# Performance work log

Hardware: AMD Instinct MI355X
Metric: run time of the kernel (lower is better)

## Reference

```python
import jax, jax.numpy as jnp
import numpy as np

B, L, R = 4, 2048, 1024        # batch, seq_len, residual_dim
HID, EXP, K = 64, 2, 3          # hidden_dim, expansion_factor, conv_kernel_size
D = HID * EXP                   # ssm_input_dim = 128
N = HID                         # SSM state size = 64


def setup_inputs() -> dict:
    key = jax.random.key(0)
    ks = jax.random.split(key, 16)
    g = lambda k, s: jax.random.normal(k, s, dtype=jnp.float32) * 0.02
    inp = {
        "up_x":   jax.random.normal(ks[0], (B, L, R), dtype=jnp.float32),
        "W_up":   g(ks[1], (R, 2 * D)),
        "b_up":   g(ks[2], (2 * D,)),
        "conv_w": g(ks[3], (D, K)),          # depthwise Conv1d weight [C,1,K] squeezed
        "conv_b": g(ks[4], (D,)),
        "W_delta": g(ks[5], (D, D)),
        "b_delta": g(ks[6], (D,)),
        "W_B":    g(ks[7], (D, N)),
        "b_B":    g(ks[8], (N,)),
        "W_C":    g(ks[9], (D, N)),
        "b_C":    g(ks[10], (N,)),
        "A_log":  jnp.log(jnp.broadcast_to(jnp.arange(1, N + 1, dtype=jnp.float32), (D, N))),
        "D_skip": jnp.ones((D,), dtype=jnp.float32),
        "W_down": g(ks[11], (D, R)),
        "b_down": g(ks[12], (R,)),
    }
    return inp


def reference(up_x, W_up, b_up, conv_w, conv_b, W_delta, b_delta,
              W_B, b_B, W_C, b_C, A_log, D_skip, W_down, b_down):
    Lq = up_x.shape[1]
    u = up_x @ W_up + b_up                               # [B,L,2D]
    left, right = jnp.split(u, 2, axis=-1)               # each [B,L,D]

    # causal depthwise conv (pad left K-1, truncate to L)
    xp = jnp.pad(left, ((0, 0), (K - 1, 0), (0, 0)))     # [B,L+K-1,D]
    conv = sum(conv_w[:, k] * xp[:, k:k + Lq, :] for k in range(K)) + conv_b
    x = jax.nn.silu(conv)                                # [B,L,D]

    # S6 selective scan
    delta = jax.nn.softplus(x @ W_delta + b_delta)       # [B,L,D]
    Bm = x @ W_B + b_B                                   # [B,L,N]
    Cm = x @ W_C + b_C                                   # [B,L,N]
    A = -jnp.exp(A_log)                                  # [D,N]
    dA = jnp.exp(delta[..., None] * A)                   # [B,L,D,N]
    dBx = delta[..., None] * Bm[:, :, None, :] * x[..., None]  # [B,L,D,N]

    def step(h, inputs):
        dA_t, dBx_t, C_t = inputs                        # [B,D,N],[B,D,N],[B,N]
        h = dA_t * h + dBx_t
        y_t = jnp.einsum('bdn,bn->bd', h, C_t)
        return h, y_t

    h0 = jnp.zeros((up_x.shape[0], D, N), dtype=x.dtype)
    _, ys = jax.lax.scan(step, h0, (jnp.swapaxes(dA, 0, 1),
                                    jnp.swapaxes(dBx, 0, 1),
                                    jnp.swapaxes(Cm, 0, 1)))
    y = jnp.swapaxes(ys, 0, 1) + D_skip * x              # [B,L,D]

    gated = y * jax.nn.silu(right)                       # SiLU gate
    return gated @ W_down + b_down                       # [B,L,R]
```

## Files before the change

kernel.cpp:

```cpp
#include <hip/hip_runtime.h>
#include <math.h>

#define B_ 4
#define L_ 2048
#define R_ 1024
#define D_ 128
#define N_ 64
#define TWO_D 256
#define M_ (B_*L_)

#define LNC 6
#define NC 64

#define LSTR 68
#define LSTRX 136

typedef __attribute__((ext_vector_type(8))) short bf16x8;
typedef __attribute__((ext_vector_type(4))) float f32x4;

__device__ __forceinline__ float silu_f(float z) {
    return z * __builtin_amdgcn_rcpf(1.0f + __expf(-z));
}

__device__ __forceinline__ float softplus_f(float z) {
    return fmaxf(z, 0.0f) + __logf(1.0f + __expf(-fabsf(z)));
}

__device__ __forceinline__ short f2bf(float f) {
    union { float f; unsigned int u; } v; v.f = f;
    unsigned int r = v.u + 0x7FFF + ((v.u >> 16) & 1);
    return (short)(r >> 16);
}

__device__ __forceinline__ bf16x8 pack8(float4 a, float4 b) {
    bf16x8 r;
    r[0] = f2bf(a.x); r[1] = f2bf(a.y); r[2] = f2bf(a.z); r[3] = f2bf(a.w);
    r[4] = f2bf(b.x); r[5] = f2bf(b.y); r[6] = f2bf(b.z); r[7] = f2bf(b.w);
    return r;
}

__global__ __launch_bounds__(256) void gemm_up_splitk(
    const float* __restrict__ A,
    const float* __restrict__ W,
    float* __restrict__ P0,
    float* __restrict__ P1)
{
    __shared__ short Al[128 * LSTR];
    __shared__ short Bl[64 * LSTR];

    int lid = blockIdx.x;
    int xcd = lid & 7;
    int slot = lid >> 3;
    int bm = xcd * 8 + (slot >> 3);
    int r3 = slot & 7;
    int bn = r3 & 3;
    int split = r3 >> 2;
    float* P = split ? P1 : P0;
    int k0 = split * 512;

    int tid = threadIdx.x;
    int w = tid >> 6, l = tid & 63;
    int lm = l & 15, q = l >> 4;
    int wm = w * 32;

    f32x4 acc[2][4];
    #pragma unroll
    for (int i = 0; i < 2; i++)
        #pragma unroll
        for (int f = 0; f < 4; f++)
            acc[i][f] = (f32x4){0.f, 0.f, 0.f, 0.f};

    int ar = tid >> 1, ak = (tid & 1) * 16;
    int bcol = tid & 63, bk = (tid >> 6) * 8;

    const float* Ag = A + (size_t)(bm * 128 + ar) * 1024 + k0 + ak;
    const float* Wg = W + (size_t)k0 * TWO_D + (size_t)bn * 64 + bcol;

    for (int kt = 0; kt < 512; kt += 32) {
        float4 a0 = *(const float4*)(Ag + kt);
        float4 a1 = *(const float4*)(Ag + kt + 4);
        float4 a2 = *(const float4*)(Ag + kt + 8);
        float4 a3 = *(const float4*)(Ag + kt + 12);
        *(bf16x8*)&Al[ar * LSTR + ak]     = pack8(a0, a1);
        *(bf16x8*)&Al[ar * LSTR + ak + 8] = pack8(a2, a3);

        float w0 = Wg[(size_t)(kt + bk + 0) * TWO_D];
        float w1 = Wg[(size_t)(kt + bk + 1) * TWO_D];
        float w2 = Wg[(size_t)(kt + bk + 2) * TWO_D];
        float w3 = Wg[(size_t)(kt + bk + 3) * TWO_D];
        float w4 = Wg[(size_t)(kt + bk + 4) * TWO_D];
        float w5 = Wg[(size_t)(kt + bk + 5) * TWO_D];
        float w6 = Wg[(size_t)(kt + bk + 6) * TWO_D];
        float w7 = Wg[(size_t)(kt + bk + 7) * TWO_D];
        *(bf16x8*)&Bl[bcol * LSTR + bk] =
            pack8(make_float4(w0, w1, w2, w3), make_float4(w4, w5, w6, w7));

        __syncthreads();

        bf16x8 af0 = *(bf16x8*)&Al[(wm + lm) * LSTR + q * 8];
        bf16x8 af1 = *(bf16x8*)&Al[(wm + 16 + lm) * LSTR + q * 8];
        bf16x8 bfr[4];
        #pragma unroll
        for (int f = 0; f < 4; f++)
            bfr[f] = *(bf16x8*)&Bl[(f * 16 + lm) * LSTR + q * 8];

        #pragma unroll
        for (int f = 0; f < 4; f++) {
            acc[0][f] = __builtin_amdgcn_mfma_f32_16x16x32_bf16(af0, bfr[f], acc[0][f], 0, 0, 0);
            acc[1][f] = __builtin_amdgcn_mfma_f32_16x16x32_bf16(af1, bfr[f], acc[1][f], 0, 0, 0);
        }

        __syncthreads();
    }

    #pragma unroll
    for (int i = 0; i < 2; i++)
        #pragma unroll
        for (int f = 0; f < 4; f++)
            #pragma unroll
            for (int e = 0; e < 4; e++) {
                int row = bm * 128 + wm + i * 16 + q * 4 + e;
                int col = bn * 64 + f * 16 + lm;
                P[(size_t)row * TWO_D + col] = acc[i][f][e];
            }
}

__global__ __launch_bounds__(256) void convproj_mfma(
    const float* __restrict__ P0,
    const float* __restrict__ P1,
    const float* __restrict__ b_up,
    const float* __restrict__ conv_w,
    const float* __restrict__ conv_b,
    const float* __restrict__ W_delta, const float* __restrict__ b_delta,
    const float* __restrict__ W_B,     const float* __restrict__ b_B,
    const float* __restrict__ W_C,     const float* __restrict__ b_C,
    float* __restrict__ x,
    float* __restrict__ u,
    float* __restrict__ delta,
    float* __restrict__ Bm,
    float* __restrict__ Cm)
{
    __shared__ float uu[66 * 128];
    __shared__ short Xl[64 * LSTRX];
    __shared__ short Bl[64 * LSTR];

    int lid = blockIdx.x;
    int xcd = lid & 7;
    int slot = lid >> 3;
    int bm = xcd * 16 + (slot >> 2);
    int bn = slot & 3;
    int tid = threadIdx.x;

    bool seq_start = (bm & 31) == 0;

    #pragma unroll
    for (int i = 0; i < 9; i++) {
        int fi = tid + i * 256;
        if (fi < 2112) {
            int row = fi >> 5;
            int c4 = (fi & 31) * 4;
            int gr = bm * 64 + row - 2;
            float4 v;
            if (seq_start && row < 2) {
                v = make_float4(0.f, 0.f, 0.f, 0.f);
            } else {
                size_t gi = (size_t)gr * TWO_D + c4;
                float4 p0 = *(const float4*)&P0[gi];
                float4 p1 = *(const float4*)&P1[gi];
                float4 bb = *(const float4*)&b_up[c4];
                v = make_float4(p0.x + p1.x + bb.x, p0.y + p1.y + bb.y,
                                p0.z + p1.z + bb.z, p0.w + p1.w + bb.w);
            }
            *(float4*)&uu[fi * 4] = v;
        }
    }

    if (bn == 1) {
        #pragma unroll
        for (int i = 0; i < 8; i++) {
            int fi = tid + i * 256;
            int row = fi >> 5;
            int c4 = (fi & 31) * 4 + 128;
            int gr = bm * 64 + row;
            size_t gi = (size_t)gr * TWO_D + c4;
            float4 p0 = *(const float4*)&P0[gi];
            float4 p1 = *(const float4*)&P1[gi];
            float4 bb = *(const float4*)&b_up[c4];
            *(float4*)&u[gi] = make_float4(p0.x + p1.x + bb.x, p0.y + p1.y + bb.y,
                                           p0.z + p1.z + bb.z, p0.w + p1.w + bb.w);
        }
    }
    __syncthreads();

    #pragma unroll
    for (int i = 0; i < 8; i++) {
        int fi = tid + i * 256;
        int row = fi >> 5;
        int c4 = (fi & 31) * 4;
        float4 v2 = *(const float4*)&uu[(row + 2) * 128 + c4];
        float4 v1 = *(const float4*)&uu[(row + 1) * 128 + c4];
        float4 v0 = *(const float4*)&uu[(row + 0) * 128 + c4];
        float4 z;
        {
            float w0 = conv_w[(c4 + 0) * 3 + 0], w1 = conv_w[(c4 + 0) * 3 + 1], w2 = conv_w[(c4 + 0) * 3 + 2];
            z.x = silu_f(fmaf(w0, v0.x, fmaf(w1, v1.x, fmaf(w2, v2.x, conv_b[c4 + 0]))));
        }
        {
            float w0 = conv_w[(c4 + 1) * 3 + 0], w1 = conv_w[(c4 + 1) * 3 + 1], w2 = conv_w[(c4 + 1) * 3 + 2];
            z.y = silu_f(fmaf(w0, v0.y, fmaf(w1, v1.y, fmaf(w2, v2.y, conv_b[c4 + 1]))));
        }
        {
            float w0 = conv_w[(c4 + 2) * 3 + 0], w1 = conv_w[(c4 + 2) * 3 + 1], w2 = conv_w[(c4 + 2) * 3 + 2];
            z.z = silu_f(fmaf(w0, v0.z, fmaf(w1, v1.z, fmaf(w2, v2.z, conv_b[c4 + 2]))));
        }
        {
            float w0 = conv_w[(c4 + 3) * 3 + 0], w1 = conv_w[(c4 + 3) * 3 + 1], w2 = conv_w[(c4 + 3) * 3 + 2];
            z.w = silu_f(fmaf(w0, v0.w, fmaf(w1, v1.w, fmaf(w2, v2.w, conv_b[c4 + 3]))));
        }
        short4 zb;
        zb.x = f2bf(z.x); zb.y = f2bf(z.y); zb.z = f2bf(z.z); zb.w = f2bf(z.w);
        *(short4*)&Xl[row * LSTRX + c4] = zb;
        if (bn == 0) {
            int gr = bm * 64 + row;
            *(float4*)&x[(size_t)gr * D_ + c4] = z;
        }
    }

    const float* Wsel; const float* bsel; int wstride;
    if (bn < 2)       { Wsel = W_delta + bn * 64; bsel = b_delta + bn * 64; wstride = 128; }
    else if (bn == 2) { Wsel = W_B;               bsel = b_B;               wstride = 64;  }
    else              { Wsel = W_C;               bsel = b_C;               wstride = 64;  }

    int w = tid >> 6, l = tid & 63;
    int lm = l & 15, q = l >> 4;
    int wm = (w & 1) * 32, wn = (w >> 1) * 32;

    f32x4 acc00 = {0,0,0,0}, acc01 = {0,0,0,0}, acc10 = {0,0,0,0}, acc11 = {0,0,0,0};

    int bcol = tid & 63, bk = (tid >> 6) * 8;
    const float* Wg = Wsel + bcol;

    __syncthreads();

    for (int kt = 0; kt < 128; kt += 32) {
        float w0 = Wg[(size_t)(kt + bk + 0) * wstride];
        float w1 = Wg[(size_t)(kt + bk + 1) * wstride];
        float w2 = Wg[(size_t)(kt + bk + 2) * wstride];
        float w3 = Wg[(size_t)(kt + bk + 3) * wstride];
        float w4 = Wg[(size_t)(kt + bk + 4) * wstride];
        float w5 = Wg[(size_t)(kt + bk + 5) * wstride];
        float w6 = Wg[(size_t)(kt + bk + 6) * wstride];
        float w7 = Wg[(size_t)(kt + bk + 7) * wstride];
        *(bf16x8*)&Bl[bcol * LSTR + bk] =
            pack8(make_float4(w0, w1, w2, w3), make_float4(w4, w5, w6, w7));

        __syncthreads();

        bf16x8 af0 = *(bf16x8*)&Xl[(wm + lm) * LSTRX + kt + q * 8];
        bf16x8 af1 = *(bf16x8*)&Xl[(wm + 16 + lm) * LSTRX + kt + q * 8];
        bf16x8 bf0 = *(bf16x8*)&Bl[(wn + lm) * LSTR + q * 8];
        bf16x8 bf1 = *(bf16x8*)&Bl[(wn + 16 + lm) * LSTR + q * 8];

        acc00 = __builtin_amdgcn_mfma_f32_16x16x32_bf16(af0, bf0, acc00, 0, 0, 0);
        acc01 = __builtin_amdgcn_mfma_f32_16x16x32_bf16(af0, bf1, acc01, 0, 0, 0);
        acc10 = __builtin_amdgcn_mfma_f32_16x16x32_bf16(af1, bf0, acc10, 0, 0, 0);
        acc11 = __builtin_amdgcn_mfma_f32_16x16x32_bf16(af1, bf1, acc11, 0, 0, 0);

        __syncthreads();
    }

    #pragma unroll
    for (int i = 0; i < 4; i++) {
        int r0 = bm * 64 + wm + q * 4 + i;
        int r1 = r0 + 16;
        int c0 = wn + lm;
        int c1 = c0 + 16;
        float v00 = acc00[i] + bsel[c0];
        float v01 = acc01[i] + bsel[c1];
        float v10 = acc10[i] + bsel[c0];
        float v11 = acc11[i] + bsel[c1];
        if (bn < 2) {
            int cc0 = bn * 64 + c0, cc1 = bn * 64 + c1;
            delta[(size_t)r0 * D_ + cc0] = softplus_f(v00);
            delta[(size_t)r0 * D_ + cc1] = softplus_f(v01);
            delta[(size_t)r1 * D_ + cc0] = softplus_f(v10);
            delta[(size_t)r1 * D_ + cc1] = softplus_f(v11);
        } else if (bn == 2) {
            Bm[(size_t)r0 * N_ + c0] = v00;
            Bm[(size_t)r0 * N_ + c1] = v01;
            Bm[(size_t)r1 * N_ + c0] = v10;
            Bm[(size_t)r1 * N_ + c1] = v11;
        } else {
            Cm[(size_t)r0 * N_ + c0] = v00;
            Cm[(size_t)r0 * N_ + c1] = v01;
            Cm[(size_t)r1 * N_ + c0] = v10;
            Cm[(size_t)r1 * N_ + c1] = v11;
        }
    }
}

__global__ __launch_bounds__(256) void scan_sumA(
    const float* __restrict__ delta,
    const float* __restrict__ x,
    const float* __restrict__ Bm,
    const float* __restrict__ A_log,
    float* __restrict__ ch_aprod,
    float* __restrict__ ch_h)
{
    constexpr int TCt = L_ >> LNC;

    int blk = blockIdx.x;
    int c = blk & (NC - 1);
    int dqg = (blk >> LNC) & 7;
    int b = blk >> (LNC + 3);
    int wv = threadIdx.x >> 6;
    int l = threadIdx.x & 63;
    int g = l >> 4, j = l & 15;
    int dq = dqg * 4 + wv;
    int d = dq * 4 + g;

    const float LOG2E = 1.44269504089f;
    float4 Ar = *(const float4*)&A_log[d * N_ + j * 4];
    float Ai0 = -__expf(Ar.x) * LOG2E;
    float Ai1 = -__expf(Ar.y) * LOG2E;
    float Ai2 = -__expf(Ar.z) * LOG2E;
    float Ai3 = -__expf(Ar.w) * LOG2E;

    size_t row0 = (size_t)b * L_ + c * TCt;
    const float* dp = delta + row0 * D_ + d;
    const float* xp = x     + row0 * D_ + d;
    const float* bp = Bm    + row0 * N_ + j * 4;

    float h0 = 0, h1 = 0, h2 = 0, h3 = 0;
    float S = 0;

    #pragma unroll 8
    for (int t = 0; t < TCt; t++) {
        float dl = dp[t * D_];
        float xv = xp[t * D_];
        float4 bv = *(const float4*)&bp[t * N_];
        float e0 = exp2f(dl * Ai0);
        float e1 = exp2f(dl * Ai1);
        float e2 = exp2f(dl * Ai2);
        float e3 = exp2f(dl * Ai3);
        float dbx = dl * xv;
        h0 = fmaf(e0, h0, dbx * bv.x);
        h1 = fmaf(e1, h1, dbx * bv.y);
        h2 = fmaf(e2, h2, dbx * bv.z);
        h3 = fmaf(e3, h3, dbx * bv.w);
        S += dl;
    }

    size_t ci = (((size_t)b * D_ + d) * NC + c) * N_ + j * 4;
    *(float4*)&ch_aprod[ci] = make_float4(exp2f(Ai0 * S), exp2f(Ai1 * S),
                                          exp2f(Ai2 * S), exp2f(Ai3 * S));
    *(float4*)&ch_h[ci]     = make_float4(h0, h1, h2, h3);
}

__global__ __launch_bounds__(256) void scan_prefix(
    float* __restrict__ aprod_hin,
    const float* __restrict__ ch_h)
{
    int idx = blockIdx.x * 256 + threadIdx.x;
    int n = idx & 63;
    int rest = idx >> 6;
    size_t base = (size_t)rest * NC * N_ + n;
    float h = 0.0f;
    #pragma unroll 8
    for (int c = 0; c < NC; c++) {
        size_t o = base + (size_t)c * N_;
        float a  = aprod_hin[o];
        float hh = ch_h[o];
        aprod_hin[o] = h;
        h = fmaf(a, h, hh);
    }
}

__global__ __launch_bounds__(256) void scan_outB(
    const float* __restrict__ delta,
    const float* __restrict__ x,
    const float* __restrict__ Bm,
    const float* __restrict__ Cm,
    const float* __restrict__ A_log,
    const float* __restrict__ D_skip,
    const float* __restrict__ hin,
    const float* __restrict__ u,
    short* __restrict__ gated)
{
    constexpr int TCt = L_ >> LNC;
    __shared__ float yl[TCt * 16];

    int blk = blockIdx.x;
    int c = blk & (NC - 1);
    int dqg = (blk >> LNC) & 7;
    int b = blk >> (LNC + 3);
    int wv = threadIdx.x >> 6;
    int l = threadIdx.x & 63;
    int g = l >> 4, j = l & 15;
    int dq = dqg * 4 + wv;
    int d = dq * 4 + g;

    const float LOG2E = 1.44269504089f;
    float4 Ar = *(const float4*)&A_log[d * N_ + j * 4];
    float Ai0 = -__expf(Ar.x) * LOG2E;
    float Ai1 = -__expf(Ar.y) * LOG2E;
    float Ai2 = -__expf(Ar.z) * LOG2E;
    float Ai3 = -__expf(Ar.w) * LOG2E;
    float dsk = D_skip[d];

    float4 hv = *(const float4*)&hin[(((size_t)b * D_ + d) * NC + c) * N_ + j * 4];
    float h0 = hv.x, h1 = hv.y, h2 = hv.z, h3 = hv.w;

    size_t row0 = (size_t)b * L_ + c * TCt;
    const float* dp = delta + row0 * D_ + d;
    const float* xp = x     + row0 * D_ + d;
    const float* bp = Bm    + row0 * N_ + j * 4;
    const float* cp = Cm    + row0 * N_ + j * 4;

    #pragma unroll 8
    for (int t = 0; t < TCt; t++) {
        float dl = dp[t * D_];
        float xv = xp[t * D_];
        float4 bv = *(const float4*)&bp[t * N_];
        float4 cv = *(const float4*)&cp[t * N_];
        float e0 = exp2f(dl * Ai0);
        float e1 = exp2f(dl * Ai1);
        float e2 = exp2f(dl * Ai2);
        float e3 = exp2f(dl * Ai3);
        float dbx = dl * xv;
        h0 = fmaf(e0, h0, dbx * bv.x);
        h1 = fmaf(e1, h1, dbx * bv.y);
        h2 = fmaf(e2, h2, dbx * bv.z);
        h3 = fmaf(e3, h3, dbx * bv.w);
        float p = fmaf(h0, cv.x, fmaf(h1, cv.y, fmaf(h2, cv.z, h3 * cv.w)));
        p += __shfl_xor(p, 1, 64);
        p += __shfl_xor(p, 2, 64);
        p += __shfl_xor(p, 4, 64);
        p += __shfl_xor(p, 8, 64);
        if (j == 0) yl[t * 16 + wv * 4 + g] = fmaf(dsk, xv, p);
    }

    __syncthreads();

    int tid = threadIdx.x;
    if (tid < 128) {
        int t = tid >> 2;
        int c4 = (tid & 3) * 4;
        size_t row = row0 + t;
        float4 yv = *(float4*)&yl[t * 16 + c4];
        float4 gv = *(const float4*)&u[row * TWO_D + 128 + dqg * 16 + c4];
        short4 o;
        o.x = f2bf(yv.x * silu_f(gv.x));
        o.y = f2bf(yv.y * silu_f(gv.y));
        o.z = f2bf(yv.z * silu_f(gv.z));
        o.w = f2bf(yv.w * silu_f(gv.w));
        *(short4*)&gated[row * D_ + dqg * 16 + c4] = o;
    }
}

__global__ __launch_bounds__(256) void gemm_down_mfma(
    const short* __restrict__ gated,
    const float* __restrict__ W,
    const float* __restrict__ bias,
    float* __restrict__ out)
{
    __shared__ short Al[64 * LSTR];
    __shared__ short Bl[64 * LSTR];

    int lid = blockIdx.x;
    int xcd = lid & 7;
    int slot = lid >> 3;
    int bm = xcd * 16 + (slot >> 4);
    int bn = slot & 15;

    int tid = threadIdx.x;
    int w = tid >> 6, l = tid & 63;
    int lm = l & 15, q = l >> 4;
    int wm = (w & 1) * 32, wn = (w >> 1) * 32;

    f32x4 acc00 = {0,0,0,0}, acc01 = {0,0,0,0}, acc10 = {0,0,0,0}, acc11 = {0,0,0,0};

    int ar = tid >> 2, ak = (tid & 3) * 8;
    int bcol = tid & 63, bk = (tid >> 6) * 8;

    const short* Gg = gated + (size_t)(bm * 64 + ar) * D_ + ak;
    const float* Wg = W + (size_t)bn * 64 + bcol;

    for (int kt = 0; kt < 128; kt += 32) {
        bf16x8 av = *(const bf16x8*)(Gg + kt);
        *(bf16x8*)&Al[ar * LSTR + ak] = av;

        float w0 = Wg[(size_t)(kt + bk + 0) * R_];
        float w1 = Wg[(size_t)(kt + bk + 1) * R_];
        float w2 = Wg[(size_t)(kt + bk + 2) * R_];
        float w3 = Wg[(size_t)(kt + bk + 3) * R_];
        float w4 = Wg[(size_t)(kt + bk + 4) * R_];
        float w5 = Wg[(size_t)(kt + bk + 5) * R_];
        float w6 = Wg[(size_t)(kt + bk + 6) * R_];
        float w7 = Wg[(size_t)(kt + bk + 7) * R_];
        *(bf16x8*)&Bl[bcol * LSTR + bk] =
            pack8(make_float4(w0, w1, w2, w3), make_float4(w4, w5, w6, w7));

        __syncthreads();

        bf16x8 af0 = *(bf16x8*)&Al[(wm + lm) * LSTR + q * 8];
        bf16x8 af1 = *(bf16x8*)&Al[(wm + 16 + lm) * LSTR + q * 8];
        bf16x8 bf0 = *(bf16x8*)&Bl[(wn + lm) * LSTR + q * 8];
        bf16x8 bf1 = *(bf16x8*)&Bl[(wn + 16 + lm) * LSTR + q * 8];

        acc00 = __builtin_amdgcn_mfma_f32_16x16x32_bf16(af0, bf0, acc00, 0, 0, 0);
        acc01 = __builtin_amdgcn_mfma_f32_16x16x32_bf16(af0, bf1, acc01, 0, 0, 0);
        acc10 = __builtin_amdgcn_mfma_f32_16x16x32_bf16(af1, bf0, acc10, 0, 0, 0);
        acc11 = __builtin_amdgcn_mfma_f32_16x16x32_bf16(af1, bf1, acc11, 0, 0, 0);

        __syncthreads();
    }

    #pragma unroll
    for (int i = 0; i < 4; i++) {
        int r0 = bm * 64 + wm + q * 4 + i;
        int r1 = r0 + 16;
        int c0 = bn * 64 + wn + lm;
        int c1 = c0 + 16;
        out[(size_t)r0 * R_ + c0] = acc00[i] + bias[c0];
        out[(size_t)r0 * R_ + c1] = acc01[i] + bias[c1];
        out[(size_t)r1 * R_ + c0] = acc10[i] + bias[c0];
        out[(size_t)r1 * R_ + c1] = acc11[i] + bias[c1];
    }
}

extern "C" void kernel_launch(void* const* d_in, const int* in_sizes, int n_in,
                              void* d_out, int out_size, void* d_ws, size_t ws_size,
                              hipStream_t stream)
{
    const float* up_x    = (const float*)d_in[0];
    const float* W_up    = (const float*)d_in[1];
    const float* b_up    = (const float*)d_in[2];
    const float* conv_w  = (const float*)d_in[3];
    const float* conv_b  = (const float*)d_in[4];
    const float* W_delta = (const float*)d_in[5];
    const float* b_delta = (const float*)d_in[6];
    const float* W_B     = (const float*)d_in[7];
    const float* b_B     = (const float*)d_in[8];
    const float* W_C     = (const float*)d_in[9];
    const float* b_C     = (const float*)d_in[10];
    const float* A_log   = (const float*)d_in[11];
    const float* D_skip  = (const float*)d_in[12];
    const float* W_down  = (const float*)d_in[13];
    const float* b_down  = (const float*)d_in[14];

    float* out = (float*)d_out;
    float* ws  = (float*)d_ws;

    float* u     = ws;
    float* x     = u + (size_t)M_ * TWO_D;
    float* delta = x + (size_t)M_ * D_;
    float* Bm    = delta + (size_t)M_ * D_;
    float* Cm    = Bm + (size_t)M_ * N_;
    float* yslot = Cm + (size_t)M_ * N_;
    float* ch_aprod = yslot + (size_t)M_ * D_;
    float* ch_h  = ch_aprod + (size_t)B_ * D_ * NC * N_;
    float* P0    = ch_h + (size_t)B_ * D_ * NC * N_;
    float* P1    = P0 + (size_t)M_ * TWO_D;
    short* gated = (short*)yslot;

    gemm_up_splitk<<<512, 256, 0, stream>>>(up_x, W_up, P0, P1);

    convproj_mfma<<<512, 256, 0, stream>>>(
        P0, P1, b_up, conv_w, conv_b,
        W_delta, b_delta, W_B, b_B, W_C, b_C,
        x, u, delta, Bm, Cm);

    scan_sumA<<<2048, 256, 0, stream>>>(
        delta, x, Bm, A_log, ch_aprod, ch_h);
    scan_prefix<<<(B_ * D_ * N_) / 256, 256, 0, stream>>>(
        ch_aprod, ch_h);
    scan_outB<<<2048, 256, 0, stream>>>(
        delta, x, Bm, Cm, A_log, D_skip, ch_aprod, u, gated);

    gemm_down_mfma<<<2048, 256, 0, stream>>>(
        gated, W_down, b_down, out);
}
```

Baseline: 210.4 us.

## Store scan intermediates in bf16 and halve scan chunk count

The x, delta, B and C intermediates written by the conv/projection kernel are now stored as bf16 instead of fp32, and the two scan kernels convert them back to float on load. This halves the memory traffic of the bandwidth-bound scan passes. The chunk count drops from 64 to 32, so each chunk covers 64 timesteps and every thread of the gating epilogue is used. The prefix kernel moves to 64-thread blocks to keep enough blocks. This costs precision in delta and the state inputs, and gives fewer, longer sequential scan blocks.

```diff
diff --git a/kernel.cpp b/kernel.cpp
--- a/kernel.cpp
+++ b/kernel.cpp
@@ -9,14 +9,15 @@
 #define TWO_D 256
 #define M_ (B_*L_)
 
-#define LNC 6
-#define NC 64
+#define LNC 5
+#define NC 32
 
 #define LSTR 68
 #define LSTRX 136
 
 typedef __attribute__((ext_vector_type(8))) short bf16x8;
 typedef __attribute__((ext_vector_type(4))) float f32x4;
+typedef __attribute__((ext_vector_type(4))) unsigned short u16x4;
 
 __device__ __forceinline__ float silu_f(float z) {
     return z * __builtin_amdgcn_rcpf(1.0f + __expf(-z));
@@ -30,6 +31,12 @@
     union { float f; unsigned int u; } v; v.f = f;
     unsigned int r = v.u + 0x7FFF + ((v.u >> 16) & 1);
     return (short)(r >> 16);
+}
+
+__device__ __forceinline__ float bf2f(unsigned short s) {
+    union { float f; unsigned int u; } v;
+    v.u = ((unsigned int)s) << 16;
+    return v.f;
 }
 
 __device__ __forceinline__ bf16x8 pack8(float4 a, float4 b) {
@@ -134,11 +141,11 @@
     const float* __restrict__ W_delta, const float* __restrict__ b_delta,
     const float* __restrict__ W_B,     const float* __restrict__ b_B,
     const float* __restrict__ W_C,     const float* __restrict__ b_C,
-    float* __restrict__ x,
+    unsigned short* __restrict__ x,
     float* __restrict__ u,
-    float* __restrict__ delta,
-    float* __restrict__ Bm,
-    float* __restrict__ Cm)
+    unsigned short* __restrict__ delta,
+    unsigned short* __restrict__ Bm,
+    unsigned short* __restrict__ Cm)
 {
     __shared__ float uu[66 * 128];
     __shared__ short Xl[64 * LSTRX];
@@ -222,7 +229,7 @@
         *(short4*)&Xl[row * LSTRX + c4] = zb;
         if (bn == 0) {
             int gr = bm * 64 + row;
-            *(float4*)&x[(size_t)gr * D_ + c4] = z;
+            *(short4*)&x[(size_t)gr * D_ + c4] = zb;
         }
     }
 
@@ -281,28 +288,28 @@
         float v11 = acc11[i] + bsel[c1];
         if (bn < 2) {
             int cc0 = bn * 64 + c0, cc1 = bn * 64 + c1;
-            delta[(size_t)r0 * D_ + cc0] = softplus_f(v00);
-            delta[(size_t)r0 * D_ + cc1] = softplus_f(v01);
-            delta[(size_t)r1 * D_ + cc0] = softplus_f(v10);
-            delta[(size_t)r1 * D_ + cc1] = softplus_f(v11);
+            delta[(size_t)r0 * D_ + cc0] = (unsigned short)f2bf(softplus_f(v00));
+            delta[(size_t)r0 * D_ + cc1] = (unsigned short)f2bf(softplus_f(v01));
+            delta[(size_t)r1 * D_ + cc0] = (unsigned short)f2bf(softplus_f(v10));
+            delta[(size_t)r1 * D_ + cc1] = (unsigned short)f2bf(softplus_f(v11));
         } else if (bn == 2) {
-            Bm[(size_t)r0 * N_ + c0] = v00;
-            Bm[(size_t)r0 * N_ + c1] = v01;
-            Bm[(size_t)r1 * N_ + c0] = v10;
-            Bm[(size_t)r1 * N_ + c1] = v11;
+            Bm[(size_t)r0 * N_ + c0] = (unsigned short)f2bf(v00);
+            Bm[(size_t)r0 * N_ + c1] = (unsigned short)f2bf(v01);
+            Bm[(size_t)r1 * N_ + c0] = (unsigned short)f2bf(v10);
+            Bm[(size_t)r1 * N_ + c1] = (unsigned short)f2bf(v11);
         } else {
-            Cm[(size_t)r0 * N_ + c0] = v00;
-            Cm[(size_t)r0 * N_ + c1] = v01;
-            Cm[(size_t)r1 * N_ + c0] = v10;
-            Cm[(size_t)r1 * N_ + c1] = v11;
+            Cm[(size_t)r0 * N_ + c0] = (unsigned short)f2bf(v00);
+            Cm[(size_t)r0 * N_ + c1] = (unsigned short)f2bf(v01);
+            Cm[(size_t)r1 * N_ + c0] = (unsigned short)f2bf(v10);
+            Cm[(size_t)r1 * N_ + c1] = (unsigned short)f2bf(v11);
         }
     }
 }
 
 __global__ __launch_bounds__(256) void scan_sumA(
-    const float* __restrict__ delta,
-    const float* __restrict__ x,
-    const float* __restrict__ Bm,
+    const unsigned short* __restrict__ delta,
+    const unsigned short* __restrict__ x,
+    const unsigned short* __restrict__ Bm,
     const float* __restrict__ A_log,
     float* __restrict__ ch_aprod,
     float* __restrict__ ch_h)
@@ -327,27 +334,27 @@
     float Ai3 = -__expf(Ar.w) * LOG2E;
 
     size_t row0 = (size_t)b * L_ + c * TCt;
-    const float* dp = delta + row0 * D_ + d;
-    const float* xp = x     + row0 * D_ + d;
-    const float* bp = Bm    + row0 * N_ + j * 4;
+    const unsigned short* dp = delta + row0 * D_ + d;
+    const unsigned short* xp = x     + row0 * D_ + d;
+    const unsigned short* bp = Bm    + row0 * N_ + j * 4;
 
     float h0 = 0, h1 = 0, h2 = 0, h3 = 0;
     float S = 0;
 
     #pragma unroll 8
     for (int t = 0; t < TCt; t++) {
-        float dl = dp[t * D_];
-        float xv = xp[t * D_];
-        float4 bv = *(const float4*)&bp[t * N_];
+        float dl = bf2f(dp[t * D_]);
+        float xv = bf2f(xp[t * D_]);
+        u16x4 bv = *(const u16x4*)&bp[t * N_];
         float e0 = exp2f(dl * Ai0);
         float e1 = exp2f(dl * Ai1);
         float e2 = exp2f(dl * Ai2);
         float e3 = exp2f(dl * Ai3);
         float dbx = dl * xv;
-        h0 = fmaf(e0, h0, dbx * bv.x);
-        h1 = fmaf(e1, h1, dbx * bv.y);
-        h2 = fmaf(e2, h2, dbx * bv.z);
-        h3 = fmaf(e3, h3, dbx * bv.w);
+        h0 = fmaf(e0, h0, dbx * bf2f(bv[0]));
+        h1 = fmaf(e1, h1, dbx * bf2f(bv[1]));
+        h2 = fmaf(e2, h2, dbx * bf2f(bv[2]));
+        h3 = fmaf(e3, h3, dbx * bf2f(bv[3]));
         S += dl;
     }
 
@@ -357,11 +364,11 @@
     *(float4*)&ch_h[ci]     = make_float4(h0, h1, h2, h3);
 }
 
-__global__ __launch_bounds__(256) void scan_prefix(
+__global__ __launch_bounds__(64) void scan_prefix(
     float* __restrict__ aprod_hin,
     const float* __restrict__ ch_h)
 {
-    int idx = blockIdx.x * 256 + threadIdx.x;
+    int idx = blockIdx.x * 64 + threadIdx.x;
     int n = idx & 63;
     int rest = idx >> 6;
     size_t base = (size_t)rest * NC * N_ + n;
@@ -377,10 +384,10 @@
 }
 
 __global__ __launch_bounds__(256) void scan_outB(
-    const float* __restrict__ delta,
-    const float* __restrict__ x,
-    const float* __restrict__ Bm,
-    const float* __restrict__ Cm,
+    const unsigned short* __restrict__ delta,
+    const unsigned short* __restrict__ x,
+    const unsigned short* __restrict__ Bm,
+    const unsigned short* __restrict__ Cm,
     const float* __restrict__ A_log,
     const float* __restrict__ D_skip,
     const float* __restrict__ hin,
@@ -412,27 +419,28 @@
     float h0 = hv.x, h1 = hv.y, h2 = hv.z, h3 = hv.w;
 
     size_t row0 = (size_t)b * L_ + c * TCt;
-    const float* dp = delta + row0 * D_ + d;
-    const float* xp = x     + row0 * D_ + d;
-    const float* bp = Bm    + row0 * N_ + j * 4;
-    const float* cp = Cm    + row0 * N_ + j * 4;
+    const unsigned short* dp = delta + row0 * D_ + d;
+    const unsigned short* xp = x     + row0 * D_ + d;
+    const unsigned short* bp = Bm    + row0 * N_ + j * 4;
+    const unsigned short* cp = Cm    + row0 * N_ + j * 4;
 
     #pragma unroll 8
     for (int t = 0; t < TCt; t++) {
-        float dl = dp[t * D_];
-        float xv = xp[t * D_];
-        float4 bv = *(const float4*)&bp[t * N_];
-        float4 cv = *(const float4*)&cp[t * N_];
+        float dl = bf2f(dp[t * D_]);
+        float xv = bf2f(xp[t * D_]);
+        u16x4 bv = *(const u16x4*)&bp[t * N_];
+        u16x4 cv = *(const u16x4*)&cp[t * N_];
         float e0 = exp2f(dl * Ai0);
         float e1 = exp2f(dl * Ai1);
         float e2 = exp2f(dl * Ai2);
         float e3 = exp2f(dl * Ai3);
         float dbx = dl * xv;
-        h0 = fmaf(e0, h0, dbx * bv.x);
-        h1 = fmaf(e1, h1, dbx * bv.y);
-        h2 = fmaf(e2, h2, dbx * bv.z);
-        h3 = fmaf(e3, h3, dbx * bv.w);
-        float p = fmaf(h0, cv.x, fmaf(h1, cv.y, fmaf(h2, cv.z, h3 * cv.w)));
+        h0 = fmaf(e0, h0, dbx * bf2f(bv[0]));
+        h1 = fmaf(e1, h1, dbx * bf2f(bv[1]));
+        h2 = fmaf(e2, h2, dbx * bf2f(bv[2]));
+        h3 = fmaf(e3, h3, dbx * bf2f(bv[3]));
+        float p = fmaf(h0, bf2f(cv[0]), fmaf(h1, bf2f(cv[1]),
+                  fmaf(h2, bf2f(cv[2]), h3 * bf2f(cv[3]))));
         p += __shfl_xor(p, 1, 64);
         p += __shfl_xor(p, 2, 64);
         p += __shfl_xor(p, 4, 64);
@@ -443,7 +451,7 @@
     __syncthreads();
 
     int tid = threadIdx.x;
-    if (tid < 128) {
+    {
         int t = tid >> 2;
         int c4 = (tid & 3) * 4;
         size_t row = row0 + t;
@@ -552,32 +560,31 @@
     float* out = (float*)d_out;
     float* ws  = (float*)d_ws;
 
-    float* u     = ws;
-    float* x     = u + (size_t)M_ * TWO_D;
-    float* delta = x + (size_t)M_ * D_;
-    float* Bm    = delta + (size_t)M_ * D_;
-    float* Cm    = Bm + (size_t)M_ * N_;
-    float* yslot = Cm + (size_t)M_ * N_;
-    float* ch_aprod = yslot + (size_t)M_ * D_;
-    float* ch_h  = ch_aprod + (size_t)B_ * D_ * NC * N_;
-    float* P0    = ch_h + (size_t)B_ * D_ * NC * N_;
-    float* P1    = P0 + (size_t)M_ * TWO_D;
-    short* gated = (short*)yslot;
+    float* u = ws;
+    unsigned short* x16     = (unsigned short*)(u + (size_t)M_ * TWO_D);
+    unsigned short* delta16 = x16     + (size_t)M_ * D_;
+    unsigned short* Bm16    = delta16 + (size_t)M_ * D_;
+    unsigned short* Cm16    = Bm16    + (size_t)M_ * N_;
+    unsigned short* gated   = Cm16    + (size_t)M_ * N_;
+    float* ch_aprod = (float*)(gated + (size_t)M_ * D_);
+    float* ch_h     = ch_aprod + (size_t)B_ * D_ * NC * N_;
+    float* P0       = ch_h     + (size_t)B_ * D_ * NC * N_;
+    float* P1       = P0       + (size_t)M_ * TWO_D;
 
     gemm_up_splitk<<<512, 256, 0, stream>>>(up_x, W_up, P0, P1);
 
     convproj_mfma<<<512, 256, 0, stream>>>(
         P0, P1, b_up, conv_w, conv_b,
         W_delta, b_delta, W_B, b_B, W_C, b_C,
-        x, u, delta, Bm, Cm);
-
-    scan_sumA<<<2048, 256, 0, stream>>>(
-        delta, x, Bm, A_log, ch_aprod, ch_h);
-    scan_prefix<<<(B_ * D_ * N_) / 256, 256, 0, stream>>>(
+        x16, u, delta16, Bm16, Cm16);
+
+    scan_sumA<<<(B_ * (D_ / 4) * NC) / 4, 256, 0, stream>>>(
+        delta16, x16, Bm16, A_log, ch_aprod, ch_h);
+    scan_prefix<<<(B_ * D_ * N_) / 64, 64, 0, stream>>>(
         ch_aprod, ch_h);
-    scan_outB<<<2048, 256, 0, stream>>>(
-        delta, x, Bm, Cm, A_log, D_skip, ch_aprod, u, gated);
+    scan_outB<<<(B_ * (D_ / 4) * NC) / 4, 256, 0, stream>>>(
+        delta16, x16, Bm16, Cm16, A_log, D_skip, ch_aprod, u, (short*)gated);
 
     gemm_down_mfma<<<2048, 256, 0, stream>>>(
-        gated, W_down, b_down, out);
-}
+        (const short*)gated, W_down, b_down, out);
+}
```

After: 237.2 us. 1.13x slower.
